# Optimization experiments

Measured on AMD Instinct MI355X. Metric: run time of the kernel, lower is better.

## Reference

```python
import jax, jax.numpy as jnp
import numpy as np
from jax import lax

N, LOOKBACK, FEAT, HID, HORIZON = 8000, 12, 64, 128, 4
DENSITY = 0.002  # ~16 avg in-degree


def setup_inputs() -> dict:
    key = jax.random.key(0)
    ks = jax.random.split(key, 20)
    tspan = jnp.arange(HORIZON, dtype=jnp.float32)
    x = jax.random.normal(ks[0], (LOOKBACK, N, FEAT), dtype=jnp.float32)
    # sparse weighted adjacency: nonzero pattern with ~DENSITY fill
    mask = (jax.random.uniform(ks[1], (N, N)) < DENSITY).astype(jnp.float32)
    adj_w = mask * jax.random.uniform(ks[2], (N, N), dtype=jnp.float32)

    def lin(k, fi, fo):
        s = 1.0 / np.sqrt(fi)
        return jax.random.uniform(k, (fi, fo), minval=-s, maxval=s, dtype=jnp.float32)

    return {
        "tspan": tspan, "x": x, "adj_w": adj_w,
        # init_enc: Linear(lookback->hid), ReLU, Linear(hid->1)
        "We1": lin(ks[3], LOOKBACK, HID), "be1": jnp.zeros((HID,), jnp.float32),
        "We2": lin(ks[4], HID, 1), "be2": jnp.zeros((1,), jnp.float32),
        # f: Linear(feat->hid), ReLU, Linear(hid->feat)
        "Wf1": lin(ks[5], FEAT, HID), "bf1": jnp.zeros((HID,), jnp.float32),
        "Wf2": lin(ks[6], HID, FEAT), "bf2": jnp.zeros((FEAT,), jnp.float32),
        # SAGEConv1 (feat->hid): lin_l (aggr, with bias), lin_r (root, no bias)
        "Wl1": lin(ks[7], FEAT, HID), "bl1": jnp.zeros((HID,), jnp.float32),
        "Wr1": lin(ks[8], FEAT, HID),
        # SAGEConv2 (hid->feat)
        "Wl2": lin(ks[9], HID, FEAT), "bl2": jnp.zeros((FEAT,), jnp.float32),
        "Wr2": lin(ks[10], HID, FEAT),
    }


def reference(tspan, x, adj_w, We1, be1, We2, be2, Wf1, bf1, Wf2, bf2,
              Wl1, bl1, Wr1, Wl2, bl2, Wr2):
    # binarized adjacency from nonzero pattern (adj.nonzero() in torch)
    A = (adj_w != 0).astype(x.dtype)                      # [N, N], edge (i,j) => msg x[i] -> node j
    deg = jnp.maximum(A.sum(axis=0), 1.0)                 # in-degree per target [N]

    def sage(h, Wl, bl, Wr):
        aggr = (A.T @ h) / deg[:, None]                   # mean over in-neighbors
        return aggr @ Wl + bl + h @ Wr

    def dxdt(h):
        x_self = jax.nn.relu(h @ Wf1 + bf1) @ Wf2 + bf2
        x_neigh = sage(jax.nn.relu(sage(h, Wl1, bl1, Wr1)), Wl2, bl2, Wr2)
        return jnp.clip(x_self + x_neigh, -1000.0, 1000.0)

    # init_enc: [L,N,F] -> permute [N,F,L] -> MLP over lookback -> [N,F]
    xe = jnp.transpose(x, (1, 2, 0))                      # [N, F, L]
    x0 = (jax.nn.relu(xe @ We1 + be1) @ We2 + be2)[..., 0]  # [N, F]

    # fixed-step Euler at tspan points (torchdiffeq method='euler')
    dts = tspan[1:] - tspan[:-1]

    def step(h, dt):
        hn = h + dt * dxdt(h)
        return hn, hn

    _, xs = lax.scan(step, x0, dts)
    return jnp.concatenate([x0[None], xs], axis=0)        # [horizon, N, F]
```

## Files before the change

kernel.cpp:

```cpp
#include <hip/hip_runtime.h>

#define N_NODES 8000
#define FEAT 64
#define HID 128
#define LOOKBACK 12
#define CAP 64

__global__ __launch_bounds__(256)
void zero_cnt_kernel(int* __restrict__ cnt) {
    int g = blockIdx.x * 256 + threadIdx.x;
    if (g < N_NODES) cnt[g] = 0;
}

__global__ __launch_bounds__(256)
void build_adj_kernel(const float* __restrict__ adj, int* __restrict__ cnt,
                      int* __restrict__ lists) {
    long q = (long)blockIdx.x * 256 + threadIdx.x;
    const long NQ = (long)N_NODES * N_NODES / 4;
    if (q >= NQ) return;
    int i  = (int)(q / (N_NODES / 4));
    int j0 = (int)(q % (N_NODES / 4)) * 4;
    float4 w = *reinterpret_cast<const float4*>(adj + (long)i * N_NODES + j0);
    float wv[4] = {w.x, w.y, w.z, w.w};
    #pragma unroll
    for (int c = 0; c < 4; ++c) {
        if (wv[c] != 0.0f) {
            int j = j0 + c;
            int p = atomicAdd(&cnt[j], 1);
            if (p < CAP) lists[(long)j * CAP + p] = i;
        }
    }
}

__global__ __launch_bounds__(256)
void prep_kernel(int* __restrict__ cnt, int* __restrict__ lists,
                 float* __restrict__ degf,
                 const float* __restrict__ Wl1, const float* __restrict__ Wr1,
                 const float* __restrict__ Wl2, const float* __restrict__ Wr2,
                 float* __restrict__ Ws1, float* __restrict__ Wc2) {
    if (blockIdx.x < 2000) {
        const int wv   = threadIdx.x >> 6;
        const int lane = threadIdx.x & 63;
        const int n = blockIdx.x * 4 + wv;
        int m = cnt[n];
        if (m > CAP) m = CAP;
        int v = (lane < m) ? lists[(long)n * CAP + lane] : 0x7FFFFFFF;
        #pragma unroll
        for (int k = 2; k <= 64; k <<= 1) {
            #pragma unroll
            for (int j = k >> 1; j > 0; j >>= 1) {
                int other = __shfl_xor(v, j);
                bool up    = ((lane & k) == 0);
                bool lower = ((lane & j) == 0);
                bool keepMin = (lower == up);
                int mn = v < other ? v : other;
                int mx = v < other ? other : v;
                v = keepMin ? mn : mx;
            }
        }
        lists[(long)n * CAP + lane] = v;
        if (lane == 0) {
            cnt[n]  = m;
            degf[n] = (float)(m > 0 ? m : 1);
        }
    } else {
        int u = (blockIdx.x - 2000) * 256 + threadIdx.x;
        if (u < 128 * 128) {
            int k = u >> 7, j = u & 127;
            Ws1[u] = (k < 64) ? Wl1[k * 128 + j] : Wr1[(k - 64) * 128 + j];
        } else if (u < 2 * 128 * 128) {
            int w = u - 128 * 128;
            int k = w >> 7, j = w & 127;
            Wc2[w] = (j < 64) ? Wl2[k * 64 + j] : Wr2[k * 64 + (j - 64)];
        }
    }
}

__global__ __launch_bounds__(256)
void init_enc_kernel(const float* __restrict__ x, const float* __restrict__ We1,
                     const float* __restrict__ be1, const float* __restrict__ We2,
                     const float* __restrict__ be2, float* __restrict__ out0) {
    __shared__ float sW1T[HID * LOOKBACK];
    __shared__ float sB1[HID];
    __shared__ float sW2[HID];
    for (int e = threadIdx.x; e < HID * LOOKBACK; e += 256) {
        int l = e / HID, h = e % HID;
        sW1T[h * LOOKBACK + l] = We1[e];
    }
    for (int e = threadIdx.x; e < HID; e += 256) { sB1[e] = be1[e]; sW2[e] = We2[e]; }
    __syncthreads();
    int g = (blockIdx.x * 256 + threadIdx.x) * 4;
    if (g >= N_NODES * FEAT) return;
    float xv[4][LOOKBACK];
    #pragma unroll
    for (int l = 0; l < LOOKBACK; ++l) {
        float4 v = *reinterpret_cast<const float4*>(x + (long)l * N_NODES * FEAT + g);
        xv[0][l] = v.x; xv[1][l] = v.y; xv[2][l] = v.z; xv[3][l] = v.w;
    }
    float b2 = be2[0];
    float acc[4] = {b2, b2, b2, b2};
    for (int h = 0; h < HID; ++h) {
        float s0 = sB1[h], s1 = s0, s2 = s0, s3 = s0;
        #pragma unroll
        for (int l = 0; l < LOOKBACK; ++l) {
            float w = sW1T[h * LOOKBACK + l];
            s0 += xv[0][l] * w; s1 += xv[1][l] * w;
            s2 += xv[2][l] * w; s3 += xv[3][l] * w;
        }
        float w2 = sW2[h];
        acc[0] += fmaxf(s0, 0.0f) * w2; acc[1] += fmaxf(s1, 0.0f) * w2;
        acc[2] += fmaxf(s2, 0.0f) * w2; acc[3] += fmaxf(s3, 0.0f) * w2;
    }
    float4 o = {acc[0], acc[1], acc[2], acc[3]};
    *reinterpret_cast<float4*>(out0 + g) = o;
}

__global__ __launch_bounds__(256)
void sageproj_kernel(const float* __restrict__ h, const int* __restrict__ lists,
                     const int* __restrict__ cnt, const float* __restrict__ degf,
                     const float* __restrict__ Ws1, const float* __restrict__ bl1,
                     const float* __restrict__ Wc2, const float* __restrict__ bl2,
                     const float* __restrict__ Wf1, const float* __restrict__ bf1,
                     const float* __restrict__ Wf2, const float* __restrict__ bf2,
                     float* __restrict__ pl, float* __restrict__ q) {
    __shared__ float v[16][132];
    __shared__ float rr[16][132];
    __shared__ float tt[16][132];
    __shared__ float xsl[16][68];
    __shared__ float wbuf[64 * 128];
    const int tid = threadIdx.x;
    const int nb = blockIdx.x * 16;
    const int ln = tid >> 4, jg = tid & 15;
    const int n = nb + ln;
    const int c0 = jg * 4;
    {
        const int f0 = c0;
        const int m = cnt[n];
        const int* l = lists + (long)n * CAP;
        const float inv = 1.0f / degf[n];
        float4 a = {0, 0, 0, 0};
        for (int e = 0; e < m; ++e) {
            float4 b = *reinterpret_cast<const float4*>(h + (long)l[e] * FEAT + f0);
            a.x += b.x; a.y += b.y; a.z += b.z; a.w += b.w;
        }
        float4 av = {a.x * inv, a.y * inv, a.z * inv, a.w * inv};
        *reinterpret_cast<float4*>(&v[ln][f0]) = av;
        *reinterpret_cast<float4*>(&v[ln][64 + f0]) =
            *reinterpret_cast<const float4*>(h + (long)n * FEAT + f0);
    }
    {
        float4 b0 = *reinterpret_cast<const float4*>(bl1 + c0);
        float4 b1 = *reinterpret_cast<const float4*>(bl1 + 64 + c0);
        float A0[4] = {b0.x, b0.y, b0.z, b0.w};
        float A1[4] = {b1.x, b1.y, b1.z, b1.w};
        for (int kc = 0; kc < 2; ++kc) {
            __syncthreads();
            for (int e = tid; e < 2048; e += 256)
                *(reinterpret_cast<float4*>(wbuf) + e) =
                    *(reinterpret_cast<const float4*>(Ws1 + kc * 8192) + e);
            __syncthreads();
            #pragma unroll 4
            for (int k = 0; k < 64; ++k) {
                float a = v[ln][kc * 64 + k];
                float4 w0 = *reinterpret_cast<const float4*>(&wbuf[k * 128 + c0]);
                float4 w1 = *reinterpret_cast<const float4*>(&wbuf[k * 128 + 64 + c0]);
                A0[0] += a * w0.x; A0[1] += a * w0.y; A0[2] += a * w0.z; A0[3] += a * w0.w;
                A1[0] += a * w1.x; A1[1] += a * w1.y; A1[2] += a * w1.z; A1[3] += a * w1.w;
            }
        }
        float4 o0 = {fmaxf(A0[0],0.f), fmaxf(A0[1],0.f), fmaxf(A0[2],0.f), fmaxf(A0[3],0.f)};
        float4 o1 = {fmaxf(A1[0],0.f), fmaxf(A1[1],0.f), fmaxf(A1[2],0.f), fmaxf(A1[3],0.f)};
        *reinterpret_cast<float4*>(&rr[ln][c0]) = o0;
        *reinterpret_cast<float4*>(&rr[ln][64 + c0]) = o1;
    }
    {
        float4 b0 = *reinterpret_cast<const float4*>(bf1 + c0);
        float4 b1 = *reinterpret_cast<const float4*>(bf1 + 64 + c0);
        float A0[4] = {b0.x, b0.y, b0.z, b0.w};
        float A1[4] = {b1.x, b1.y, b1.z, b1.w};
        __syncthreads();
        for (int e = tid; e < 2048; e += 256)
            *(reinterpret_cast<float4*>(wbuf) + e) =
                *(reinterpret_cast<const float4*>(Wf1) + e);
        __syncthreads();
        #pragma unroll 4
        for (int k = 0; k < 64; ++k) {
            float a = v[ln][64 + k];
            float4 w0 = *reinterpret_cast<const float4*>(&wbuf[k * 128 + c0]);
            float4 w1 = *reinterpret_cast<const float4*>(&wbuf[k * 128 + 64 + c0]);
            A0[0] += a * w0.x; A0[1] += a * w0.y; A0[2] += a * w0.z; A0[3] += a * w0.w;
            A1[0] += a * w1.x; A1[1] += a * w1.y; A1[2] += a * w1.z; A1[3] += a * w1.w;
        }
        float4 o0 = {fmaxf(A0[0],0.f), fmaxf(A0[1],0.f), fmaxf(A0[2],0.f), fmaxf(A0[3],0.f)};
        float4 o1 = {fmaxf(A1[0],0.f), fmaxf(A1[1],0.f), fmaxf(A1[2],0.f), fmaxf(A1[3],0.f)};
        *reinterpret_cast<float4*>(&tt[ln][c0]) = o0;
        *reinterpret_cast<float4*>(&tt[ln][64 + c0]) = o1;
    }
    {
        float4 b0 = *reinterpret_cast<const float4*>(bf2 + c0);
        float X[4] = {b0.x, b0.y, b0.z, b0.w};
        __syncthreads();
        for (int e = tid; e < 2048; e += 256)
            *(reinterpret_cast<float4*>(wbuf) + e) =
                *(reinterpret_cast<const float4*>(Wf2) + e);
        __syncthreads();
        #pragma unroll 4
        for (int k = 0; k < 128; ++k) {
            float a = tt[ln][k];
            float4 w = *reinterpret_cast<const float4*>(&wbuf[k * 64 + c0]);
            X[0] += a * w.x; X[1] += a * w.y; X[2] += a * w.z; X[3] += a * w.w;
        }
        float4 o = {X[0], X[1], X[2], X[3]};
        *reinterpret_cast<float4*>(&xsl[ln][c0]) = o;
    }
    {
        float P0[4] = {0, 0, 0, 0};
        float P1[4] = {0, 0, 0, 0};
        for (int kc = 0; kc < 2; ++kc) {
            __syncthreads();
            for (int e = tid; e < 2048; e += 256)
                *(reinterpret_cast<float4*>(wbuf) + e) =
                    *(reinterpret_cast<const float4*>(Wc2 + kc * 8192) + e);
            __syncthreads();
            #pragma unroll 4
            for (int k = 0; k < 64; ++k) {
                float a = rr[ln][kc * 64 + k];
                float4 w0 = *reinterpret_cast<const float4*>(&wbuf[k * 128 + c0]);
                float4 w1 = *reinterpret_cast<const float4*>(&wbuf[k * 128 + 64 + c0]);
                P0[0] += a * w0.x; P0[1] += a * w0.y; P0[2] += a * w0.z; P0[3] += a * w0.w;
                P1[0] += a * w1.x; P1[1] += a * w1.y; P1[2] += a * w1.z; P1[3] += a * w1.w;
            }
        }
        float4 op = {P0[0], P0[1], P0[2], P0[3]};
        *reinterpret_cast<float4*>(pl + (long)n * FEAT + c0) = op;
        float4 bv = *reinterpret_cast<const float4*>(bl2 + c0);
        float4 oq = {P1[0] + bv.x + xsl[ln][c0 + 0],
                     P1[1] + bv.y + xsl[ln][c0 + 1],
                     P1[2] + bv.z + xsl[ln][c0 + 2],
                     P1[3] + bv.w + xsl[ln][c0 + 3]};
        *reinterpret_cast<float4*>(q + (long)n * FEAT + c0) = oq;
    }
}

__global__ __launch_bounds__(256)
void epi_kernel(const float* __restrict__ pl, const float* __restrict__ q,
                const int* __restrict__ lists, const int* __restrict__ cnt,
                const float* __restrict__ degf, const float* __restrict__ hcur,
                const float* __restrict__ tspan, int step,
                float* __restrict__ hnext) {
    const int tid = threadIdx.x;
    const int ln = tid >> 4, sub = tid & 15;
    const int n = blockIdx.x * 16 + ln;
    const int f0 = sub * 4;
    const int m = cnt[n];
    const int* l = lists + (long)n * CAP;
    const float inv = 1.0f / degf[n];
    float4 a = {0, 0, 0, 0};
    for (int e = 0; e < m; ++e) {
        float4 b = *reinterpret_cast<const float4*>(pl + (long)l[e] * FEAT + f0);
        a.x += b.x; a.y += b.y; a.z += b.z; a.w += b.w;
    }
    const float dt = tspan[step + 1] - tspan[step];
    float4 qv = *reinterpret_cast<const float4*>(q + (long)n * FEAT + f0);
    float4 hv = *reinterpret_cast<const float4*>(hcur + (long)n * FEAT + f0);
    float s0 = qv.x + a.x * inv, s1 = qv.y + a.y * inv;
    float s2 = qv.z + a.z * inv, s3 = qv.w + a.w * inv;
    s0 = fminf(fmaxf(s0, -1000.f), 1000.f); s1 = fminf(fmaxf(s1, -1000.f), 1000.f);
    s2 = fminf(fmaxf(s2, -1000.f), 1000.f); s3 = fminf(fmaxf(s3, -1000.f), 1000.f);
    float4 o = {hv.x + dt * s0, hv.y + dt * s1, hv.z + dt * s2, hv.w + dt * s3};
    *reinterpret_cast<float4*>(hnext + (long)n * FEAT + f0) = o;
}

extern "C" void kernel_launch(void* const* d_in, const int* in_sizes, int n_in,
                              void* d_out, int out_size, void* d_ws, size_t ws_size,
                              hipStream_t stream) {
    const float* tspan = (const float*)d_in[0];
    const float* x     = (const float*)d_in[1];
    const float* adj   = (const float*)d_in[2];
    const float* We1   = (const float*)d_in[3];
    const float* be1   = (const float*)d_in[4];
    const float* We2   = (const float*)d_in[5];
    const float* be2   = (const float*)d_in[6];
    const float* Wf1   = (const float*)d_in[7];
    const float* bf1   = (const float*)d_in[8];
    const float* Wf2   = (const float*)d_in[9];
    const float* bf2   = (const float*)d_in[10];
    const float* Wl1   = (const float*)d_in[11];
    const float* bl1   = (const float*)d_in[12];
    const float* Wr1   = (const float*)d_in[13];
    const float* Wl2   = (const float*)d_in[14];
    const float* bl2   = (const float*)d_in[15];
    const float* Wr2   = (const float*)d_in[16];
    float* out = (float*)d_out;

    char* ws = (char*)d_ws;
    int*   lists = (int*)  (ws + 0);
    int*   cnt   = (int*)  (ws + 2048000);
    float* degf  = (float*)(ws + 2080000);
    float* Ws1   = (float*)(ws + 2112000);
    float* Wc2   = (float*)(ws + 2177536);
    float* pl    = (float*)(ws + 2243072);
    float* q     = (float*)(ws + 4291072);

    zero_cnt_kernel<<<32, 256, 0, stream>>>(cnt);
    build_adj_kernel<<<62500, 256, 0, stream>>>(adj, cnt, lists);
    prep_kernel<<<2128, 256, 0, stream>>>(cnt, lists, degf, Wl1, Wr1, Wl2, Wr2, Ws1, Wc2);
    init_enc_kernel<<<500, 256, 0, stream>>>(x, We1, be1, We2, be2, out);

    for (int s = 0; s < 3; ++s) {
        const float* hcur  = out + (long)s       * N_NODES * FEAT;
        float*       hnext = out + (long)(s + 1) * N_NODES * FEAT;
        sageproj_kernel<<<500, 256, 0, stream>>>(hcur, lists, cnt, degf,
                                                 Ws1, bl1, Wc2, bl2,
                                                 Wf1, bf1, Wf2, bf2, pl, q);
        epi_kernel<<<500, 256, 0, stream>>>(pl, q, lists, cnt, degf, hcur, tspan, s, hnext);
    }
}
```

Before: 250.2 us.

## Register-tile sageproj GEMMs over 32 nodes with transposed activations in LDS

The fused SAGE/MLP projection kernel now handles 32 nodes per block instead of 16. Activations are transposed into LDS so each thread computes a 4x4 register tile (4 nodes by 4 output columns), with weights read straight from global/L2 instead of being staged through LDS behind repeated barriers. The aim is more FMAs per load and far fewer syncthreads. The trade-offs are half the grid (250 blocks on a large GPU, so under one block per CU), a larger LDS pool and higher register pressure.

```diff
diff --git a/kernel.cpp b/kernel.cpp
--- a/kernel.cpp
+++ b/kernel.cpp
@@ -50,9 +50,7 @@
             #pragma unroll
             for (int j = k >> 1; j > 0; j >>= 1) {
                 int other = __shfl_xor(v, j);
-                bool up    = ((lane & k) == 0);
-                bool lower = ((lane & j) == 0);
-                bool keepMin = (lower == up);
+                bool keepMin = (((lane & j) == 0) == ((lane & k) == 0));
                 int mn = v < other ? v : other;
                 int mx = v < other ? other : v;
                 v = keepMin ? mn : mx;
@@ -123,122 +121,171 @@
                      const float* __restrict__ Wf1, const float* __restrict__ bf1,
                      const float* __restrict__ Wf2, const float* __restrict__ bf2,
                      float* __restrict__ pl, float* __restrict__ q) {
-    __shared__ float v[16][132];
-    __shared__ float rr[16][132];
-    __shared__ float tt[16][132];
-    __shared__ float xsl[16][68];
-    __shared__ float wbuf[64 * 128];
+    __shared__ __align__(16) char pool[64512];
+    float (*vT)[36]   = reinterpret_cast<float(*)[36]>(pool);
+    float (*rrT)[36]  = reinterpret_cast<float(*)[36]>(pool + 18432);
+    float (*ttT)[36]  = reinterpret_cast<float(*)[36]>(pool + 36864);
+    float (*xslT)[36] = reinterpret_cast<float(*)[36]>(pool + 55296);
+    float (*v)[132]   = reinterpret_cast<float(*)[132]>(pool + 18432);
+
     const int tid = threadIdx.x;
-    const int nb = blockIdx.x * 16;
-    const int ln = tid >> 4, jg = tid & 15;
-    const int n = nb + ln;
-    const int c0 = jg * 4;
-    {
-        const int f0 = c0;
+    const int nb = blockIdx.x * 32;
+    {
+        const int ln = tid >> 3, sub = tid & 7;
+        const int n = nb + ln;
+        const int f0 = sub * 8;
         const int m = cnt[n];
         const int* l = lists + (long)n * CAP;
         const float inv = 1.0f / degf[n];
-        float4 a = {0, 0, 0, 0};
+        float acc[8] = {0, 0, 0, 0, 0, 0, 0, 0};
         for (int e = 0; e < m; ++e) {
-            float4 b = *reinterpret_cast<const float4*>(h + (long)l[e] * FEAT + f0);
-            a.x += b.x; a.y += b.y; a.z += b.z; a.w += b.w;
-        }
-        float4 av = {a.x * inv, a.y * inv, a.z * inv, a.w * inv};
-        *reinterpret_cast<float4*>(&v[ln][f0]) = av;
-        *reinterpret_cast<float4*>(&v[ln][64 + f0]) =
-            *reinterpret_cast<const float4*>(h + (long)n * FEAT + f0);
-    }
-    {
-        float4 b0 = *reinterpret_cast<const float4*>(bl1 + c0);
-        float4 b1 = *reinterpret_cast<const float4*>(bl1 + 64 + c0);
-        float A0[4] = {b0.x, b0.y, b0.z, b0.w};
-        float A1[4] = {b1.x, b1.y, b1.z, b1.w};
-        for (int kc = 0; kc < 2; ++kc) {
-            __syncthreads();
-            for (int e = tid; e < 2048; e += 256)
-                *(reinterpret_cast<float4*>(wbuf) + e) =
-                    *(reinterpret_cast<const float4*>(Ws1 + kc * 8192) + e);
-            __syncthreads();
-            #pragma unroll 4
-            for (int k = 0; k < 64; ++k) {
-                float a = v[ln][kc * 64 + k];
-                float4 w0 = *reinterpret_cast<const float4*>(&wbuf[k * 128 + c0]);
-                float4 w1 = *reinterpret_cast<const float4*>(&wbuf[k * 128 + 64 + c0]);
-                A0[0] += a * w0.x; A0[1] += a * w0.y; A0[2] += a * w0.z; A0[3] += a * w0.w;
-                A1[0] += a * w1.x; A1[1] += a * w1.y; A1[2] += a * w1.z; A1[3] += a * w1.w;
-            }
-        }
-        float4 o0 = {fmaxf(A0[0],0.f), fmaxf(A0[1],0.f), fmaxf(A0[2],0.f), fmaxf(A0[3],0.f)};
-        float4 o1 = {fmaxf(A1[0],0.f), fmaxf(A1[1],0.f), fmaxf(A1[2],0.f), fmaxf(A1[3],0.f)};
-        *reinterpret_cast<float4*>(&rr[ln][c0]) = o0;
-        *reinterpret_cast<float4*>(&rr[ln][64 + c0]) = o1;
-    }
-    {
-        float4 b0 = *reinterpret_cast<const float4*>(bf1 + c0);
-        float4 b1 = *reinterpret_cast<const float4*>(bf1 + 64 + c0);
-        float A0[4] = {b0.x, b0.y, b0.z, b0.w};
-        float A1[4] = {b1.x, b1.y, b1.z, b1.w};
-        __syncthreads();
-        for (int e = tid; e < 2048; e += 256)
-            *(reinterpret_cast<float4*>(wbuf) + e) =
-                *(reinterpret_cast<const float4*>(Wf1) + e);
-        __syncthreads();
+            const float* hp = h + (long)l[e] * FEAT + f0;
+            float4 b0 = *reinterpret_cast<const float4*>(hp);
+            float4 b1 = *reinterpret_cast<const float4*>(hp + 4);
+            acc[0] += b0.x; acc[1] += b0.y; acc[2] += b0.z; acc[3] += b0.w;
+            acc[4] += b1.x; acc[5] += b1.y; acc[6] += b1.z; acc[7] += b1.w;
+        }
+        float4 a0 = {acc[0] * inv, acc[1] * inv, acc[2] * inv, acc[3] * inv};
+        float4 a1 = {acc[4] * inv, acc[5] * inv, acc[6] * inv, acc[7] * inv};
+        *reinterpret_cast<float4*>(&v[ln][f0])     = a0;
+        *reinterpret_cast<float4*>(&v[ln][f0 + 4]) = a1;
+        const float* hn = h + (long)n * FEAT + f0;
+        *reinterpret_cast<float4*>(&v[ln][64 + f0])     = *reinterpret_cast<const float4*>(hn);
+        *reinterpret_cast<float4*>(&v[ln][64 + f0 + 4]) = *reinterpret_cast<const float4*>(hn + 4);
+    }
+    __syncthreads();
+    {
+        const int k = tid & 127;
+        const int no = (tid >> 7) * 16;
+        float t0[16];
+        #pragma unroll
+        for (int j = 0; j < 16; ++j) t0[j] = v[no + j][k];
+        #pragma unroll
+        for (int i = 0; i < 4; ++i) {
+            float4 o = {t0[4*i], t0[4*i+1], t0[4*i+2], t0[4*i+3]};
+            *reinterpret_cast<float4*>(&vT[k][no + 4*i]) = o;
+        }
+    }
+    __syncthreads();
+    const int jg = tid >> 3, lng = tid & 7;
+    const int c0 = jg * 4, n0 = lng * 4;
+    {
+        float acc[4][4];
+        #pragma unroll
+        for (int c = 0; c < 4; ++c) {
+            float b = bl1[c0 + c];
+            #pragma unroll
+            for (int n = 0; n < 4; ++n) acc[c][n] = b;
+        }
+        #pragma unroll 4
+        for (int k = 0; k < 128; ++k) {
+            float4 a = *reinterpret_cast<const float4*>(&vT[k][n0]);
+            float4 w = *reinterpret_cast<const float4*>(Ws1 + k * 128 + c0);
+            float av[4] = {a.x, a.y, a.z, a.w};
+            float wv[4] = {w.x, w.y, w.z, w.w};
+            #pragma unroll
+            for (int c = 0; c < 4; ++c)
+                #pragma unroll
+                for (int n = 0; n < 4; ++n)
+                    acc[c][n] += av[n] * wv[c];
+        }
+        #pragma unroll
+        for (int c = 0; c < 4; ++c) {
+            float4 o = {fmaxf(acc[c][0],0.f), fmaxf(acc[c][1],0.f),
+                        fmaxf(acc[c][2],0.f), fmaxf(acc[c][3],0.f)};
+            *reinterpret_cast<float4*>(&rrT[c0 + c][n0]) = o;
+        }
+    }
+    {
+        float acc[4][4];
+        #pragma unroll
+        for (int c = 0; c < 4; ++c) {
+            float b = bf1[c0 + c];
+            #pragma unroll
+            for (int n = 0; n < 4; ++n) acc[c][n] = b;
+        }
         #pragma unroll 4
         for (int k = 0; k < 64; ++k) {
-            float a = v[ln][64 + k];
-            float4 w0 = *reinterpret_cast<const float4*>(&wbuf[k * 128 + c0]);
-            float4 w1 = *reinterpret_cast<const float4*>(&wbuf[k * 128 + 64 + c0]);
-            A0[0] += a * w0.x; A0[1] += a * w0.y; A0[2] += a * w0.z; A0[3] += a * w0.w;
-            A1[0] += a * w1.x; A1[1] += a * w1.y; A1[2] += a * w1.z; A1[3] += a * w1.w;
-        }
-        float4 o0 = {fmaxf(A0[0],0.f), fmaxf(A0[1],0.f), fmaxf(A0[2],0.f), fmaxf(A0[3],0.f)};
-        float4 o1 = {fmaxf(A1[0],0.f), fmaxf(A1[1],0.f), fmaxf(A1[2],0.f), fmaxf(A1[3],0.f)};
-        *reinterpret_cast<float4*>(&tt[ln][c0]) = o0;
-        *reinterpret_cast<float4*>(&tt[ln][64 + c0]) = o1;
-    }
-    {
-        float4 b0 = *reinterpret_cast<const float4*>(bf2 + c0);
-        float X[4] = {b0.x, b0.y, b0.z, b0.w};
-        __syncthreads();
-        for (int e = tid; e < 2048; e += 256)
-            *(reinterpret_cast<float4*>(wbuf) + e) =
-                *(reinterpret_cast<const float4*>(Wf2) + e);
-        __syncthreads();
+            float4 a = *reinterpret_cast<const float4*>(&vT[64 + k][n0]);
+            float4 w = *reinterpret_cast<const float4*>(Wf1 + k * 128 + c0);
+            float av[4] = {a.x, a.y, a.z, a.w};
+            float wv[4] = {w.x, w.y, w.z, w.w};
+            #pragma unroll
+            for (int c = 0; c < 4; ++c)
+                #pragma unroll
+                for (int n = 0; n < 4; ++n)
+                    acc[c][n] += av[n] * wv[c];
+        }
+        #pragma unroll
+        for (int c = 0; c < 4; ++c) {
+            float4 o = {fmaxf(acc[c][0],0.f), fmaxf(acc[c][1],0.f),
+                        fmaxf(acc[c][2],0.f), fmaxf(acc[c][3],0.f)};
+            *reinterpret_cast<float4*>(&ttT[c0 + c][n0]) = o;
+        }
+    }
+    __syncthreads();
+    if (jg < 16) {
+        float acc[4][4];
+        #pragma unroll
+        for (int c = 0; c < 4; ++c) {
+            float b = bf2[c0 + c];
+            #pragma unroll
+            for (int n = 0; n < 4; ++n) acc[c][n] = b;
+        }
         #pragma unroll 4
         for (int k = 0; k < 128; ++k) {
-            float a = tt[ln][k];
-            float4 w = *reinterpret_cast<const float4*>(&wbuf[k * 64 + c0]);
-            X[0] += a * w.x; X[1] += a * w.y; X[2] += a * w.z; X[3] += a * w.w;
-        }
-        float4 o = {X[0], X[1], X[2], X[3]};
-        *reinterpret_cast<float4*>(&xsl[ln][c0]) = o;
-    }
-    {
-        float P0[4] = {0, 0, 0, 0};
-        float P1[4] = {0, 0, 0, 0};
-        for (int kc = 0; kc < 2; ++kc) {
-            __syncthreads();
-            for (int e = tid; e < 2048; e += 256)
-                *(reinterpret_cast<float4*>(wbuf) + e) =
-                    *(reinterpret_cast<const float4*>(Wc2 + kc * 8192) + e);
-            __syncthreads();
-            #pragma unroll 4
-            for (int k = 0; k < 64; ++k) {
-                float a = rr[ln][kc * 64 + k];
-                float4 w0 = *reinterpret_cast<const float4*>(&wbuf[k * 128 + c0]);
-                float4 w1 = *reinterpret_cast<const float4*>(&wbuf[k * 128 + 64 + c0]);
-                P0[0] += a * w0.x; P0[1] += a * w0.y; P0[2] += a * w0.z; P0[3] += a * w0.w;
-                P1[0] += a * w1.x; P1[1] += a * w1.y; P1[2] += a * w1.z; P1[3] += a * w1.w;
+            float4 a = *reinterpret_cast<const float4*>(&ttT[k][n0]);
+            float4 w = *reinterpret_cast<const float4*>(Wf2 + k * 64 + c0);
+            float av[4] = {a.x, a.y, a.z, a.w};
+            float wv[4] = {w.x, w.y, w.z, w.w};
+            #pragma unroll
+            for (int c = 0; c < 4; ++c)
+                #pragma unroll
+                for (int n = 0; n < 4; ++n)
+                    acc[c][n] += av[n] * wv[c];
+        }
+        #pragma unroll
+        for (int c = 0; c < 4; ++c) {
+            float4 o = {acc[c][0], acc[c][1], acc[c][2], acc[c][3]};
+            *reinterpret_cast<float4*>(&xslT[c0 + c][n0]) = o;
+        }
+    }
+    __syncthreads();
+    {
+        float acc[4][4];
+        #pragma unroll
+        for (int c = 0; c < 4; ++c)
+            #pragma unroll
+            for (int n = 0; n < 4; ++n) acc[c][n] = 0.0f;
+        #pragma unroll 4
+        for (int k = 0; k < 128; ++k) {
+            float4 a = *reinterpret_cast<const float4*>(&rrT[k][n0]);
+            float4 w = *reinterpret_cast<const float4*>(Wc2 + k * 128 + c0);
+            float av[4] = {a.x, a.y, a.z, a.w};
+            float wv[4] = {w.x, w.y, w.z, w.w};
+            #pragma unroll
+            for (int c = 0; c < 4; ++c)
+                #pragma unroll
+                for (int n = 0; n < 4; ++n)
+                    acc[c][n] += av[n] * wv[c];
+        }
+        if (jg < 16) {
+            #pragma unroll
+            for (int n = 0; n < 4; ++n) {
+                float4 o = {acc[0][n], acc[1][n], acc[2][n], acc[3][n]};
+                *reinterpret_cast<float4*>(pl + (long)(nb + n0 + n) * FEAT + c0) = o;
             }
-        }
-        float4 op = {P0[0], P0[1], P0[2], P0[3]};
-        *reinterpret_cast<float4*>(pl + (long)n * FEAT + c0) = op;
-        float4 bv = *reinterpret_cast<const float4*>(bl2 + c0);
-        float4 oq = {P1[0] + bv.x + xsl[ln][c0 + 0],
-                     P1[1] + bv.y + xsl[ln][c0 + 1],
-                     P1[2] + bv.z + xsl[ln][c0 + 2],
-                     P1[3] + bv.w + xsl[ln][c0 + 3]};
-        *reinterpret_cast<float4*>(q + (long)n * FEAT + c0) = oq;
+        } else {
+            const int cq = c0 - 64;
+            #pragma unroll
+            for (int n = 0; n < 4; ++n) {
+                float4 o = {acc[0][n] + bl2[cq + 0] + xslT[cq + 0][n0 + n],
+                            acc[1][n] + bl2[cq + 1] + xslT[cq + 1][n0 + n],
+                            acc[2][n] + bl2[cq + 2] + xslT[cq + 2][n0 + n],
+                            acc[3][n] + bl2[cq + 3] + xslT[cq + 3][n0 + n]};
+                *reinterpret_cast<float4*>(q + (long)(nb + n0 + n) * FEAT + cq) = o;
+            }
+        }
     }
 }
 
@@ -310,7 +357,7 @@
     for (int s = 0; s < 3; ++s) {
         const float* hcur  = out + (long)s       * N_NODES * FEAT;
         float*       hnext = out + (long)(s + 1) * N_NODES * FEAT;
-        sageproj_kernel<<<500, 256, 0, stream>>>(hcur, lists, cnt, degf,
+        sageproj_kernel<<<250, 256, 0, stream>>>(hcur, lists, cnt, degf,
                                                  Ws1, bl1, Wc2, bl2,
                                                  Wf1, bf1, Wf2, bf2, pl, q);
         epi_kernel<<<500, 256, 0, stream>>>(pl, q, lists, cnt, degf, hcur, tspan, s, hnext);
```

After: 303.8 us. +21.4%, slower.

## Fuse prep, encoder and Euler steps into one persistent kernel with grid barriers

Applied to the files above, without the earlier changes.

Merges the prep, init-encoder, sageproj and epilogue kernels into a single persistent kernel of 500 blocks, with a software grid-wide barrier built on global atomics in place of the kernel boundaries. The aim is to remove the launch and drain gaps between the roughly eight small launches. The barrier needs all 500 blocks to be resident at once, which launch_bounds(256,2) and the shared-memory use have to allow. The spin loop gives up after a fixed iteration count, so if blocks are not co-resident it can produce wrong results instead of hanging.

```diff
diff --git a/kernel.cpp b/kernel.cpp
--- a/kernel.cpp
+++ b/kernel.cpp
@@ -5,11 +5,13 @@
 #define HID 128
 #define LOOKBACK 12
 #define CAP 64
+#define NBLK 500
 
 __global__ __launch_bounds__(256)
-void zero_cnt_kernel(int* __restrict__ cnt) {
+void zero_kernel(int* __restrict__ cnt, unsigned* __restrict__ bar) {
     int g = blockIdx.x * 256 + threadIdx.x;
     if (g < N_NODES) cnt[g] = 0;
+    if (g < 32) bar[g] = 0u;
 }
 
 __global__ __launch_bounds__(256)
@@ -32,243 +34,252 @@
     }
 }
 
-__global__ __launch_bounds__(256)
-void prep_kernel(int* __restrict__ cnt, int* __restrict__ lists,
+__device__ __forceinline__ void gsync(unsigned* __restrict__ bar) {
+    __syncthreads();
+    if (threadIdx.x == 0) {
+        __threadfence();
+        unsigned g = __hip_atomic_load(&bar[16], __ATOMIC_RELAXED, __HIP_MEMORY_SCOPE_AGENT);
+        unsigned a = __hip_atomic_fetch_add(&bar[0], 1u, __ATOMIC_ACQ_REL, __HIP_MEMORY_SCOPE_AGENT);
+        if (a == (unsigned)(NBLK - 1)) {
+            __hip_atomic_store(&bar[0], 0u, __ATOMIC_RELAXED, __HIP_MEMORY_SCOPE_AGENT);
+            __hip_atomic_fetch_add(&bar[16], 1u, __ATOMIC_RELEASE, __HIP_MEMORY_SCOPE_AGENT);
+        } else {
+            long it = 0;
+            while (__hip_atomic_load(&bar[16], __ATOMIC_ACQUIRE, __HIP_MEMORY_SCOPE_AGENT) == g) {
+                if (++it > (1L << 23)) break;
+            }
+        }
+    }
+    __syncthreads();
+    __threadfence();
+}
+
+__global__ __launch_bounds__(256, 2)
+void mega_kernel(const float* __restrict__ tspan, const float* __restrict__ x,
+                 const float* __restrict__ We1, const float* __restrict__ be1,
+                 const float* __restrict__ We2, const float* __restrict__ be2,
+                 const float* __restrict__ Wf1, const float* __restrict__ bf1,
+                 const float* __restrict__ Wf2, const float* __restrict__ bf2,
+                 const float* __restrict__ Wl1, const float* __restrict__ bl1,
+                 const float* __restrict__ Wr1,
+                 const float* __restrict__ Wl2, const float* __restrict__ bl2,
+                 const float* __restrict__ Wr2,
+                 int* __restrict__ cnt, int* __restrict__ lists,
                  float* __restrict__ degf,
-                 const float* __restrict__ Wl1, const float* __restrict__ Wr1,
-                 const float* __restrict__ Wl2, const float* __restrict__ Wr2,
-                 float* __restrict__ Ws1, float* __restrict__ Wc2) {
-    if (blockIdx.x < 2000) {
-        const int wv   = threadIdx.x >> 6;
-        const int lane = threadIdx.x & 63;
-        const int n = blockIdx.x * 4 + wv;
-        int m = cnt[n];
-        if (m > CAP) m = CAP;
-        int v = (lane < m) ? lists[(long)n * CAP + lane] : 0x7FFFFFFF;
-        #pragma unroll
-        for (int k = 2; k <= 64; k <<= 1) {
-            #pragma unroll
-            for (int j = k >> 1; j > 0; j >>= 1) {
-                int other = __shfl_xor(v, j);
-                bool up    = ((lane & k) == 0);
-                bool lower = ((lane & j) == 0);
-                bool keepMin = (lower == up);
-                int mn = v < other ? v : other;
-                int mx = v < other ? other : v;
-                v = keepMin ? mn : mx;
-            }
-        }
-        lists[(long)n * CAP + lane] = v;
-        if (lane == 0) {
-            cnt[n]  = m;
-            degf[n] = (float)(m > 0 ? m : 1);
-        }
-    } else {
-        int u = (blockIdx.x - 2000) * 256 + threadIdx.x;
-        if (u < 128 * 128) {
-            int k = u >> 7, j = u & 127;
-            Ws1[u] = (k < 64) ? Wl1[k * 128 + j] : Wr1[(k - 64) * 128 + j];
-        } else if (u < 2 * 128 * 128) {
-            int w = u - 128 * 128;
-            int k = w >> 7, j = w & 127;
-            Wc2[w] = (j < 64) ? Wl2[k * 64 + j] : Wr2[k * 64 + (j - 64)];
-        }
-    }
-}
-
-__global__ __launch_bounds__(256)
-void init_enc_kernel(const float* __restrict__ x, const float* __restrict__ We1,
-                     const float* __restrict__ be1, const float* __restrict__ We2,
-                     const float* __restrict__ be2, float* __restrict__ out0) {
-    __shared__ float sW1T[HID * LOOKBACK];
-    __shared__ float sB1[HID];
-    __shared__ float sW2[HID];
-    for (int e = threadIdx.x; e < HID * LOOKBACK; e += 256) {
-        int l = e / HID, h = e % HID;
-        sW1T[h * LOOKBACK + l] = We1[e];
-    }
-    for (int e = threadIdx.x; e < HID; e += 256) { sB1[e] = be1[e]; sW2[e] = We2[e]; }
-    __syncthreads();
-    int g = (blockIdx.x * 256 + threadIdx.x) * 4;
-    if (g >= N_NODES * FEAT) return;
-    float xv[4][LOOKBACK];
-    #pragma unroll
-    for (int l = 0; l < LOOKBACK; ++l) {
-        float4 v = *reinterpret_cast<const float4*>(x + (long)l * N_NODES * FEAT + g);
-        xv[0][l] = v.x; xv[1][l] = v.y; xv[2][l] = v.z; xv[3][l] = v.w;
-    }
-    float b2 = be2[0];
-    float acc[4] = {b2, b2, b2, b2};
-    for (int h = 0; h < HID; ++h) {
-        float s0 = sB1[h], s1 = s0, s2 = s0, s3 = s0;
-        #pragma unroll
-        for (int l = 0; l < LOOKBACK; ++l) {
-            float w = sW1T[h * LOOKBACK + l];
-            s0 += xv[0][l] * w; s1 += xv[1][l] * w;
-            s2 += xv[2][l] * w; s3 += xv[3][l] * w;
-        }
-        float w2 = sW2[h];
-        acc[0] += fmaxf(s0, 0.0f) * w2; acc[1] += fmaxf(s1, 0.0f) * w2;
-        acc[2] += fmaxf(s2, 0.0f) * w2; acc[3] += fmaxf(s3, 0.0f) * w2;
-    }
-    float4 o = {acc[0], acc[1], acc[2], acc[3]};
-    *reinterpret_cast<float4*>(out0 + g) = o;
-}
-
-__global__ __launch_bounds__(256)
-void sageproj_kernel(const float* __restrict__ h, const int* __restrict__ lists,
-                     const int* __restrict__ cnt, const float* __restrict__ degf,
-                     const float* __restrict__ Ws1, const float* __restrict__ bl1,
-                     const float* __restrict__ Wc2, const float* __restrict__ bl2,
-                     const float* __restrict__ Wf1, const float* __restrict__ bf1,
-                     const float* __restrict__ Wf2, const float* __restrict__ bf2,
-                     float* __restrict__ pl, float* __restrict__ q) {
+                 float* __restrict__ Ws1, float* __restrict__ Wc2,
+                 float* __restrict__ pl, float* __restrict__ q,
+                 float* __restrict__ out, unsigned* __restrict__ bar) {
     __shared__ float v[16][132];
     __shared__ float rr[16][132];
     __shared__ float tt[16][132];
     __shared__ float xsl[16][68];
     __shared__ float wbuf[64 * 128];
     const int tid = threadIdx.x;
-    const int nb = blockIdx.x * 16;
+    const int bid = blockIdx.x;
+
+    {
+        const int wv = tid >> 6, lane = tid & 63;
+        #pragma unroll 1
+        for (int r = 0; r < 4; ++r) {
+            const int n = (bid * 4 + wv) + 2000 * r;
+            int m = cnt[n]; if (m > CAP) m = CAP;
+            int val = (lane < m) ? lists[(long)n * CAP + lane] : 0x7FFFFFFF;
+            #pragma unroll
+            for (int k = 2; k <= 64; k <<= 1) {
+                #pragma unroll
+                for (int j = k >> 1; j > 0; j >>= 1) {
+                    int other = __shfl_xor(val, j);
+                    bool keepMin = (((lane & j) == 0) == ((lane & k) == 0));
+                    int mn = val < other ? val : other;
+                    int mx = val < other ? other : val;
+                    val = keepMin ? mn : mx;
+                }
+            }
+            lists[(long)n * CAP + lane] = val;
+            if (lane == 0) { cnt[n] = m; degf[n] = (float)(m > 0 ? m : 1); }
+        }
+        const int gid = bid * 256 + tid;
+        for (int u = gid; u < 2 * 128 * 128; u += 128000) {
+            if (u < 128 * 128) {
+                int k = u >> 7, j = u & 127;
+                Ws1[u] = (k < 64) ? Wl1[k * 128 + j] : Wr1[(k - 64) * 128 + j];
+            } else {
+                int w = u - 128 * 128;
+                int k = w >> 7, j = w & 127;
+                Wc2[w] = (j < 64) ? Wl2[k * 64 + j] : Wr2[k * 64 + (j - 64)];
+            }
+        }
+        float* sW1T = wbuf;
+        float* sB1  = wbuf + 1536;
+        float* sW2  = wbuf + 1664;
+        __syncthreads();
+        for (int e = tid; e < HID * LOOKBACK; e += 256) {
+            int l = e / HID, hh = e % HID;
+            sW1T[hh * LOOKBACK + l] = We1[e];
+        }
+        for (int e = tid; e < HID; e += 256) { sB1[e] = be1[e]; sW2[e] = We2[e]; }
+        __syncthreads();
+        int g = (bid * 256 + tid) * 4;
+        float xv[4][LOOKBACK];
+        #pragma unroll
+        for (int l = 0; l < LOOKBACK; ++l) {
+            float4 vv = *reinterpret_cast<const float4*>(x + (long)l * N_NODES * FEAT + g);
+            xv[0][l] = vv.x; xv[1][l] = vv.y; xv[2][l] = vv.z; xv[3][l] = vv.w;
+        }
+        float b2 = be2[0];
+        float acc[4] = {b2, b2, b2, b2};
+        for (int hh = 0; hh < HID; ++hh) {
+            float s0 = sB1[hh], s1 = s0, s2 = s0, s3 = s0;
+            #pragma unroll
+            for (int l = 0; l < LOOKBACK; ++l) {
+                float w = sW1T[hh * LOOKBACK + l];
+                s0 += xv[0][l] * w; s1 += xv[1][l] * w;
+                s2 += xv[2][l] * w; s3 += xv[3][l] * w;
+            }
+            float w2 = sW2[hh];
+            acc[0] += fmaxf(s0, 0.0f) * w2; acc[1] += fmaxf(s1, 0.0f) * w2;
+            acc[2] += fmaxf(s2, 0.0f) * w2; acc[3] += fmaxf(s3, 0.0f) * w2;
+        }
+        float4 o = {acc[0], acc[1], acc[2], acc[3]};
+        *reinterpret_cast<float4*>(out + g) = o;
+    }
+    gsync(bar);
+
     const int ln = tid >> 4, jg = tid & 15;
-    const int n = nb + ln;
+    const int nb = bid * 16;
+    const int n  = nb + ln;
     const int c0 = jg * 4;
-    {
-        const int f0 = c0;
-        const int m = cnt[n];
-        const int* l = lists + (long)n * CAP;
-        const float inv = 1.0f / degf[n];
-        float4 a = {0, 0, 0, 0};
-        for (int e = 0; e < m; ++e) {
-            float4 b = *reinterpret_cast<const float4*>(h + (long)l[e] * FEAT + f0);
-            a.x += b.x; a.y += b.y; a.z += b.z; a.w += b.w;
-        }
-        float4 av = {a.x * inv, a.y * inv, a.z * inv, a.w * inv};
-        *reinterpret_cast<float4*>(&v[ln][f0]) = av;
-        *reinterpret_cast<float4*>(&v[ln][64 + f0]) =
-            *reinterpret_cast<const float4*>(h + (long)n * FEAT + f0);
-    }
-    {
-        float4 b0 = *reinterpret_cast<const float4*>(bl1 + c0);
-        float4 b1 = *reinterpret_cast<const float4*>(bl1 + 64 + c0);
-        float A0[4] = {b0.x, b0.y, b0.z, b0.w};
-        float A1[4] = {b1.x, b1.y, b1.z, b1.w};
-        for (int kc = 0; kc < 2; ++kc) {
+    for (int s = 0; s < 3; ++s) {
+        const float* h     = out + (long)s * N_NODES * FEAT;
+        float*       hnext = out + (long)(s + 1) * N_NODES * FEAT;
+        {
+            const int m = cnt[n];
+            const int* l = lists + (long)n * CAP;
+            const float inv = 1.0f / degf[n];
+            float4 a = {0, 0, 0, 0};
+            for (int e = 0; e < m; ++e) {
+                float4 b = *reinterpret_cast<const float4*>(h + (long)l[e] * FEAT + c0);
+                a.x += b.x; a.y += b.y; a.z += b.z; a.w += b.w;
+            }
+            float4 av = {a.x * inv, a.y * inv, a.z * inv, a.w * inv};
+            *reinterpret_cast<float4*>(&v[ln][c0]) = av;
+            *reinterpret_cast<float4*>(&v[ln][64 + c0]) =
+                *reinterpret_cast<const float4*>(h + (long)n * FEAT + c0);
+        }
+        {
+            float4 b0 = *reinterpret_cast<const float4*>(bl1 + c0);
+            float4 b1 = *reinterpret_cast<const float4*>(bl1 + 64 + c0);
+            float A0[4] = {b0.x, b0.y, b0.z, b0.w};
+            float A1[4] = {b1.x, b1.y, b1.z, b1.w};
+            for (int kc = 0; kc < 2; ++kc) {
+                __syncthreads();
+                for (int e = tid; e < 2048; e += 256)
+                    *(reinterpret_cast<float4*>(wbuf) + e) =
+                        *(reinterpret_cast<const float4*>(Ws1 + kc * 8192) + e);
+                __syncthreads();
+                #pragma unroll 4
+                for (int k = 0; k < 64; ++k) {
+                    float a = v[ln][kc * 64 + k];
+                    float4 w0 = *reinterpret_cast<const float4*>(&wbuf[k * 128 + c0]);
+                    float4 w1 = *reinterpret_cast<const float4*>(&wbuf[k * 128 + 64 + c0]);
+                    A0[0] += a * w0.x; A0[1] += a * w0.y; A0[2] += a * w0.z; A0[3] += a * w0.w;
+                    A1[0] += a * w1.x; A1[1] += a * w1.y; A1[2] += a * w1.z; A1[3] += a * w1.w;
+                }
+            }
+            float4 o0 = {fmaxf(A0[0],0.f), fmaxf(A0[1],0.f), fmaxf(A0[2],0.f), fmaxf(A0[3],0.f)};
+            float4 o1 = {fmaxf(A1[0],0.f), fmaxf(A1[1],0.f), fmaxf(A1[2],0.f), fmaxf(A1[3],0.f)};
+            *reinterpret_cast<float4*>(&rr[ln][c0]) = o0;
+            *reinterpret_cast<float4*>(&rr[ln][64 + c0]) = o1;
+        }
+        {
+            float4 b0 = *reinterpret_cast<const float4*>(bf1 + c0);
+            float4 b1 = *reinterpret_cast<const float4*>(bf1 + 64 + c0);
+            float A0[4] = {b0.x, b0.y, b0.z, b0.w};
+            float A1[4] = {b1.x, b1.y, b1.z, b1.w};
             __syncthreads();
             for (int e = tid; e < 2048; e += 256)
                 *(reinterpret_cast<float4*>(wbuf) + e) =
-                    *(reinterpret_cast<const float4*>(Ws1 + kc * 8192) + e);
+                    *(reinterpret_cast<const float4*>(Wf1) + e);
             __syncthreads();
             #pragma unroll 4
             for (int k = 0; k < 64; ++k) {
-                float a = v[ln][kc * 64 + k];
+                float a = v[ln][64 + k];
                 float4 w0 = *reinterpret_cast<const float4*>(&wbuf[k * 128 + c0]);
                 float4 w1 = *reinterpret_cast<const float4*>(&wbuf[k * 128 + 64 + c0]);
                 A0[0] += a * w0.x; A0[1] += a * w0.y; A0[2] += a * w0.z; A0[3] += a * w0.w;
                 A1[0] += a * w1.x; A1[1] += a * w1.y; A1[2] += a * w1.z; A1[3] += a * w1.w;
             }
-        }
-        float4 o0 = {fmaxf(A0[0],0.f), fmaxf(A0[1],0.f), fmaxf(A0[2],0.f), fmaxf(A0[3],0.f)};
-        float4 o1 = {fmaxf(A1[0],0.f), fmaxf(A1[1],0.f), fmaxf(A1[2],0.f), fmaxf(A1[3],0.f)};
-        *reinterpret_cast<float4*>(&rr[ln][c0]) = o0;
-        *reinterpret_cast<float4*>(&rr[ln][64 + c0]) = o1;
-    }
-    {
-        float4 b0 = *reinterpret_cast<const float4*>(bf1 + c0);
-        float4 b1 = *reinterpret_cast<const float4*>(bf1 + 64 + c0);
-        float A0[4] = {b0.x, b0.y, b0.z, b0.w};
-        float A1[4] = {b1.x, b1.y, b1.z, b1.w};
-        __syncthreads();
-        for (int e = tid; e < 2048; e += 256)
-            *(reinterpret_cast<float4*>(wbuf) + e) =
-                *(reinterpret_cast<const float4*>(Wf1) + e);
-        __syncthreads();
-        #pragma unroll 4
-        for (int k = 0; k < 64; ++k) {
-            float a = v[ln][64 + k];
-            float4 w0 = *reinterpret_cast<const float4*>(&wbuf[k * 128 + c0]);
-            float4 w1 = *reinterpret_cast<const float4*>(&wbuf[k * 128 + 64 + c0]);
-            A0[0] += a * w0.x; A0[1] += a * w0.y; A0[2] += a * w0.z; A0[3] += a * w0.w;
-            A1[0] += a * w1.x; A1[1] += a * w1.y; A1[2] += a * w1.z; A1[3] += a * w1.w;
-        }
-        float4 o0 = {fmaxf(A0[0],0.f), fmaxf(A0[1],0.f), fmaxf(A0[2],0.f), fmaxf(A0[3],0.f)};
-        float4 o1 = {fmaxf(A1[0],0.f), fmaxf(A1[1],0.f), fmaxf(A1[2],0.f), fmaxf(A1[3],0.f)};
-        *reinterpret_cast<float4*>(&tt[ln][c0]) = o0;
-        *reinterpret_cast<float4*>(&tt[ln][64 + c0]) = o1;
-    }
-    {
-        float4 b0 = *reinterpret_cast<const float4*>(bf2 + c0);
-        float X[4] = {b0.x, b0.y, b0.z, b0.w};
-        __syncthreads();
-        for (int e = tid; e < 2048; e += 256)
-            *(reinterpret_cast<float4*>(wbuf) + e) =
-                *(reinterpret_cast<const float4*>(Wf2) + e);
-        __syncthreads();
-        #pragma unroll 4
-        for (int k = 0; k < 128; ++k) {
-            float a = tt[ln][k];
-            float4 w = *reinterpret_cast<const float4*>(&wbuf[k * 64 + c0]);
-            X[0] += a * w.x; X[1] += a * w.y; X[2] += a * w.z; X[3] += a * w.w;
-        }
-        float4 o = {X[0], X[1], X[2], X[3]};
-        *reinterpret_cast<float4*>(&xsl[ln][c0]) = o;
-    }
-    {
-        float P0[4] = {0, 0, 0, 0};
-        float P1[4] = {0, 0, 0, 0};
-        for (int kc = 0; kc < 2; ++kc) {
+            float4 o0 = {fmaxf(A0[0],0.f), fmaxf(A0[1],0.f), fmaxf(A0[2],0.f), fmaxf(A0[3],0.f)};
+            float4 o1 = {fmaxf(A1[0],0.f), fmaxf(A1[1],0.f), fmaxf(A1[2],0.f), fmaxf(A1[3],0.f)};
+            *reinterpret_cast<float4*>(&tt[ln][c0]) = o0;
+            *reinterpret_cast<float4*>(&tt[ln][64 + c0]) = o1;
+        }
+        {
+            float4 b0 = *reinterpret_cast<const float4*>(bf2 + c0);
+            float X[4] = {b0.x, b0.y, b0.z, b0.w};
             __syncthreads();
             for (int e = tid; e < 2048; e += 256)
                 *(reinterpret_cast<float4*>(wbuf) + e) =
-                    *(reinterpret_cast<const float4*>(Wc2 + kc * 8192) + e);
+                    *(reinterpret_cast<const float4*>(Wf2) + e);
             __syncthreads();
             #pragma unroll 4
-            for (int k = 0; k < 64; ++k) {
-                float a = rr[ln][kc * 64 + k];
-                float4 w0 = *reinterpret_cast<const float4*>(&wbuf[k * 128 + c0]);
-                float4 w1 = *reinterpret_cast<const float4*>(&wbuf[k * 128 + 64 + c0]);
-                P0[0] += a * w0.x; P0[1] += a * w0.y; P0[2] += a * w0.z; P0[3] += a * w0.w;
-                P1[0] += a * w1.x; P1[1] += a * w1.y; P1[2] += a * w1.z; P1[3] += a * w1.w;
-            }
-        }
-        float4 op = {P0[0], P0[1], P0[2], P0[3]};
-        *reinterpret_cast<float4*>(pl + (long)n * FEAT + c0) = op;
-        float4 bv = *reinterpret_cast<const float4*>(bl2 + c0);
-        float4 oq = {P1[0] + bv.x + xsl[ln][c0 + 0],
-                     P1[1] + bv.y + xsl[ln][c0 + 1],
-                     P1[2] + bv.z + xsl[ln][c0 + 2],
-                     P1[3] + bv.w + xsl[ln][c0 + 3]};
-        *reinterpret_cast<float4*>(q + (long)n * FEAT + c0) = oq;
+            for (int k = 0; k < 128; ++k) {
+                float a = tt[ln][k];
+                float4 w = *reinterpret_cast<const float4*>(&wbuf[k * 64 + c0]);
+                X[0] += a * w.x; X[1] += a * w.y; X[2] += a * w.z; X[3] += a * w.w;
+            }
+            float4 o = {X[0], X[1], X[2], X[3]};
+            *reinterpret_cast<float4*>(&xsl[ln][c0]) = o;
+        }
+        {
+            float P0[4] = {0, 0, 0, 0};
+            float P1[4] = {0, 0, 0, 0};
+            for (int kc = 0; kc < 2; ++kc) {
+                __syncthreads();
+                for (int e = tid; e < 2048; e += 256)
+                    *(reinterpret_cast<float4*>(wbuf) + e) =
+                        *(reinterpret_cast<const float4*>(Wc2 + kc * 8192) + e);
+                __syncthreads();
+                #pragma unroll 4
+                for (int k = 0; k < 64; ++k) {
+                    float a = rr[ln][kc * 64 + k];
+                    float4 w0 = *reinterpret_cast<const float4*>(&wbuf[k * 128 + c0]);
+                    float4 w1 = *reinterpret_cast<const float4*>(&wbuf[k * 128 + 64 + c0]);
+                    P0[0] += a * w0.x; P0[1] += a * w0.y; P0[2] += a * w0.z; P0[3] += a * w0.w;
+                    P1[0] += a * w1.x; P1[1] += a * w1.y; P1[2] += a * w1.z; P1[3] += a * w1.w;
+                }
+            }
+            float4 op = {P0[0], P0[1], P0[2], P0[3]};
+            *reinterpret_cast<float4*>(pl + (long)n * FEAT + c0) = op;
+            float4 bv = *reinterpret_cast<const float4*>(bl2 + c0);
+            float4 oq = {P1[0] + bv.x + xsl[ln][c0 + 0],
+                         P1[1] + bv.y + xsl[ln][c0 + 1],
+                         P1[2] + bv.z + xsl[ln][c0 + 2],
+                         P1[3] + bv.w + xsl[ln][c0 + 3]};
+            *reinterpret_cast<float4*>(q + (long)n * FEAT + c0) = oq;
+        }
+        gsync(bar);
+        {
+            const int m = cnt[n];
+            const int* l = lists + (long)n * CAP;
+            const float inv = 1.0f / degf[n];
+            float4 a = {0, 0, 0, 0};
+            for (int e = 0; e < m; ++e) {
+                float4 b = *reinterpret_cast<const float4*>(pl + (long)l[e] * FEAT + c0);
+                a.x += b.x; a.y += b.y; a.z += b.z; a.w += b.w;
+            }
+            const float dt = tspan[s + 1] - tspan[s];
+            float4 qv = *reinterpret_cast<const float4*>(q + (long)n * FEAT + c0);
+            float4 hv = *reinterpret_cast<const float4*>(h + (long)n * FEAT + c0);
+            float s0 = qv.x + a.x * inv, s1 = qv.y + a.y * inv;
+            float s2 = qv.z + a.z * inv, s3 = qv.w + a.w * inv;
+            s0 = fminf(fmaxf(s0, -1000.f), 1000.f); s1 = fminf(fmaxf(s1, -1000.f), 1000.f);
+            s2 = fminf(fmaxf(s2, -1000.f), 1000.f); s3 = fminf(fmaxf(s3, -1000.f), 1000.f);
+            float4 o = {hv.x + dt * s0, hv.y + dt * s1, hv.z + dt * s2, hv.w + dt * s3};
+            *reinterpret_cast<float4*>(hnext + (long)n * FEAT + c0) = o;
+        }
+        if (s < 2) gsync(bar);
     }
-}
-
-__global__ __launch_bounds__(256)
-void epi_kernel(const float* __restrict__ pl, const float* __restrict__ q,
-                const int* __restrict__ lists, const int* __restrict__ cnt,
-                const float* __restrict__ degf, const float* __restrict__ hcur,
-                const float* __restrict__ tspan, int step,
-                float* __restrict__ hnext) {
-    const int tid = threadIdx.x;
-    const int ln = tid >> 4, sub = tid & 15;
-    const int n = blockIdx.x * 16 + ln;
-    const int f0 = sub * 4;
-    const int m = cnt[n];
-    const int* l = lists + (long)n * CAP;
-    const float inv = 1.0f / degf[n];
-    float4 a = {0, 0, 0, 0};
-    for (int e = 0; e < m; ++e) {
-        float4 b = *reinterpret_cast<const float4*>(pl + (long)l[e] * FEAT + f0);
-        a.x += b.x; a.y += b.y; a.z += b.z; a.w += b.w;
-    }
-    const float dt = tspan[step + 1] - tspan[step];
-    float4 qv = *reinterpret_cast<const float4*>(q + (long)n * FEAT + f0);
-    float4 hv = *reinterpret_cast<const float4*>(hcur + (long)n * FEAT + f0);
-    float s0 = qv.x + a.x * inv, s1 = qv.y + a.y * inv;
-    float s2 = qv.z + a.z * inv, s3 = qv.w + a.w * inv;
-    s0 = fminf(fmaxf(s0, -1000.f), 1000.f); s1 = fminf(fmaxf(s1, -1000.f), 1000.f);
-    s2 = fminf(fmaxf(s2, -1000.f), 1000.f); s3 = fminf(fmaxf(s3, -1000.f), 1000.f);
-    float4 o = {hv.x + dt * s0, hv.y + dt * s1, hv.z + dt * s2, hv.w + dt * s3};
-    *reinterpret_cast<float4*>(hnext + (long)n * FEAT + f0) = o;
 }
 
 extern "C" void kernel_launch(void* const* d_in, const int* in_sizes, int n_in,
@@ -294,25 +305,20 @@
     float* out = (float*)d_out;
 
     char* ws = (char*)d_ws;
-    int*   lists = (int*)  (ws + 0);
-    int*   cnt   = (int*)  (ws + 2048000);
-    float* degf  = (float*)(ws + 2080000);
-    float* Ws1   = (float*)(ws + 2112000);
-    float* Wc2   = (float*)(ws + 2177536);
-    float* pl    = (float*)(ws + 2243072);
-    float* q     = (float*)(ws + 4291072);
-
-    zero_cnt_kernel<<<32, 256, 0, stream>>>(cnt);
+    int*      lists = (int*)     (ws + 0);
+    int*      cnt   = (int*)     (ws + 2048000);
+    float*    degf  = (float*)   (ws + 2080000);
+    float*    Ws1   = (float*)   (ws + 2112000);
+    float*    Wc2   = (float*)   (ws + 2177536);
+    float*    pl    = (float*)   (ws + 2243072);
+    float*    q     = (float*)   (ws + 4291072);
+    unsigned* bar   = (unsigned*)(ws + 6339072);
+
+    zero_kernel<<<32, 256, 0, stream>>>(cnt, bar);
     build_adj_kernel<<<62500, 256, 0, stream>>>(adj, cnt, lists);
-    prep_kernel<<<2128, 256, 0, stream>>>(cnt, lists, degf, Wl1, Wr1, Wl2, Wr2, Ws1, Wc2);
-    init_enc_kernel<<<500, 256, 0, stream>>>(x, We1, be1, We2, be2, out);
-
-    for (int s = 0; s < 3; ++s) {
-        const float* hcur  = out + (long)s       * N_NODES * FEAT;
-        float*       hnext = out + (long)(s + 1) * N_NODES * FEAT;
-        sageproj_kernel<<<500, 256, 0, stream>>>(hcur, lists, cnt, degf,
-                                                 Ws1, bl1, Wc2, bl2,
-                                                 Wf1, bf1, Wf2, bf2, pl, q);
-        epi_kernel<<<500, 256, 0, stream>>>(pl, q, lists, cnt, degf, hcur, tspan, s, hnext);
-    }
-}
+    mega_kernel<<<NBLK, 256, 0, stream>>>(tspan, x, We1, be1, We2, be2,
+                                          Wf1, bf1, Wf2, bf2,
+                                          Wl1, bl1, Wr1, Wl2, bl2, Wr2,
+                                          cnt, lists, degf, Ws1, Wc2,
+                                          pl, q, out, bar);
+}
```

Result: slower. 917.1 us (+266.5%).
